# Performance work log

Hardware: AMD Instinct MI355X
Metric: run time of the kernel (lower is better)

Reference implementation:

```python
import jax, jax.numpy as jnp
import numpy as np
import math

B, L, C, H = 8, 1024, 1024, 8
EPS = 1e-5

def setup_inputs() -> dict:
    key = jax.random.key(0)
    ks = jax.random.split(key, 5)
    s = 0.02
    return {
        "x": jax.random.normal(ks[0], (B, L, C), dtype=jnp.float32),
        "ln_g": jnp.ones((C,), dtype=jnp.float32),
        "ln_b": jnp.zeros((C,), dtype=jnp.float32),
        "w_qkv": jax.random.normal(ks[1], (C, 3 * C), dtype=jnp.float32) * s,
        "b_qkv": jax.random.normal(ks[2], (3 * C,), dtype=jnp.float32) * s,
        "w_out": jax.random.normal(ks[3], (C, C), dtype=jnp.float32) * s,
        "b_out": jax.random.normal(ks[4], (C,), dtype=jnp.float32) * s,
    }

def reference(x, ln_g, ln_b, w_qkv, b_qkv, w_out, b_out):
    bs, length, width = x.shape
    ch = width // H
    # LayerNorm over channels
    mu = jnp.mean(x, axis=-1, keepdims=True)
    var = jnp.mean(jnp.square(x - mu), axis=-1, keepdims=True)
    xn = (x - mu) * jax.lax.rsqrt(var + EPS) * ln_g + ln_b
    # fused QKV projection
    qkv = jnp.einsum('blc,cd->bld', xn, w_qkv) + b_qkv  # [B, L, 3C]
    q, k, v = jnp.split(qkv, 3, axis=2)                 # each [B, L, C]
    scale = 1.0 / math.sqrt(math.sqrt(ch))
    # faithful raw row-major reshape as in the torch .view call
    q = (q * scale).reshape(bs * H, length, ch)
    k = (k * scale).reshape(bs * H, length, ch)
    v = v.reshape(bs * H, length, ch)
    w = jnp.einsum('bqc,bkc->bqk', q, k)                # [B*H, L, L] score matrix
    w = jax.nn.softmax(w.astype(jnp.float32), axis=-1).astype(q.dtype)
    attn = jnp.einsum('bqk,bkc->bqc', w, v).reshape(bs, length, -1)
    out = jnp.einsum('blc,cd->bld', attn, w_out) + b_out + xn  # residual uses normalized x
    return out
```

## Files before the change

### kernel.cpp

```cpp
#include <hip/hip_runtime.h>
#include <hip/hip_bf16.h>


typedef __attribute__((ext_vector_type(8))) short short8;
typedef __attribute__((ext_vector_type(4))) float f32x4;

#define QK_SCALE 0.29730177875068026f

__device__ __forceinline__ float bf2f(ushort u) {
    union { float f; unsigned int i; } c; c.i = ((unsigned int)u) << 16; return c.f;
}
__device__ __forceinline__ ushort f2bf(float f) {
    union { float f; unsigned int i; } c; c.f = f;
    unsigned int x = c.i;
    return (ushort)((x + 0x7FFFu + ((x >> 16) & 1u)) >> 16);
}

__device__ __forceinline__ void gload_lds16(const ushort* g, ushort* l) {
    __builtin_amdgcn_global_load_lds(
        (const __attribute__((address_space(1))) unsigned int*)g,
        (__attribute__((address_space(3))) unsigned int*)l, 16, 0, 0);
}

__global__ __launch_bounds__(256) void ln_kernel(
    const float* __restrict__ x, const float* __restrict__ g,
    const float* __restrict__ b, ushort* __restrict__ xn) {
    int row = blockIdx.x;
    int tid = threadIdx.x;
    const float* xr = x + (size_t)row * 1024;
    float4 v4 = *(const float4*)(xr + tid * 4);
    float v[4] = {v4.x, v4.y, v4.z, v4.w};
    float s1 = 0.f, s2 = 0.f;
#pragma unroll
    for (int j = 0; j < 4; j++) { s1 += v[j]; s2 += v[j] * v[j]; }
#pragma unroll
    for (int m = 32; m >= 1; m >>= 1) { s1 += __shfl_xor(s1, m); s2 += __shfl_xor(s2, m); }
    __shared__ float r1[4], r2[4];
    int lane = tid & 63, w = tid >> 6;
    if (lane == 0) { r1[w] = s1; r2[w] = s2; }
    __syncthreads();
    s1 = r1[0] + r1[1] + r1[2] + r1[3];
    s2 = r2[0] + r2[1] + r2[2] + r2[3];
    float mu = s1 * (1.0f / 1024.0f);
    float var = s2 * (1.0f / 1024.0f) - mu * mu;
    float rs = rsqrtf(var + 1e-5f);
    int c0 = tid * 4;
    float4 gg = *(const float4*)(g + c0);
    float4 bb = *(const float4*)(b + c0);
    float gA[4] = {gg.x, gg.y, gg.z, gg.w};
    float bA[4] = {bb.x, bb.y, bb.z, bb.w};
    ushort o[4];
#pragma unroll
    for (int j = 0; j < 4; j++) o[j] = f2bf((v[j] - mu) * rs * gA[j] + bA[j]);
    uint2 pk;
    pk.x = (uint)o[0] | ((uint)o[1] << 16);
    pk.y = (uint)o[2] | ((uint)o[3] << 16);
    *(uint2*)(xn + (size_t)row * 1024 + c0) = pk;
}

__global__ __launch_bounds__(256) void transpose_kernel(
    const float* __restrict__ in, ushort* __restrict__ out, int R, int Cc) {
    __shared__ ushort t[32][33];
    int bx = blockIdx.x * 32, by = blockIdx.y * 32;
    int tx = threadIdx.x & 31, ty = threadIdx.x >> 5;
#pragma unroll
    for (int j = 0; j < 32; j += 8)
        t[ty + j][tx] = f2bf(in[(size_t)(by + ty + j) * Cc + bx + tx]);
    __syncthreads();
#pragma unroll
    for (int j = 0; j < 32; j += 8)
        out[(size_t)(bx + ty + j) * R + by + tx] = t[tx][ty + j];
}

__global__ __launch_bounds__(256) void transpose_head(
    const ushort* __restrict__ in, ushort* __restrict__ out) {
    __shared__ ushort t[32][33];
    int h = blockIdx.z;
    int j0 = blockIdx.y * 32;
    int d0 = blockIdx.x * 32;
    int tx = threadIdx.x & 31, ty = threadIdx.x >> 5;
    const ushort* src = in + (size_t)h * 131072;
    ushort* dst = out + (size_t)h * 131072;
#pragma unroll
    for (int j = 0; j < 32; j += 8)
        t[ty + j][tx] = src[(size_t)(j0 + ty + j) * 128 + d0 + tx];
    __syncthreads();
#pragma unroll
    for (int j = 0; j < 32; j += 8)
        dst[(size_t)(d0 + ty + j) * 1024 + j0 + tx] = t[tx][ty + j];
}

__global__ __launch_bounds__(256) void gemm_qkv(
    const ushort* __restrict__ A, const ushort* __restrict__ Bt,
    const float* __restrict__ bias, ushort* __restrict__ out0,
    ushort* __restrict__ out1, ushort* __restrict__ out2) {
    const int K = 1024;
    __shared__ __align__(16) ushort As[128 * 64];
    __shared__ __align__(16) ushort Bs[128 * 64];

    int tid = threadIdx.x;
    int lane = tid & 63, w = tid >> 6;
    int l15 = lane & 15, q4 = lane >> 4;
    int wr = (w >> 1) * 64, wc = (w & 1) * 64;
    int rowBase = blockIdx.y * 128, colBase = blockIdx.x * 128;

    f32x4 acc[4][4];
    f32x4 zero = {0.f, 0.f, 0.f, 0.f};
#pragma unroll
    for (int mi = 0; mi < 4; mi++)
#pragma unroll
        for (int ni = 0; ni < 4; ni++) acc[mi][ni] = zero;

    for (int kt = 0; kt < 16; kt++) {
        __syncthreads();
#pragma unroll
        for (int i = 0; i < 4; i++) {
            int linear = i * 256 + w * 64 + lane;
            int r = linear >> 3, p = linear & 7;
            int l = p ^ (r & 7);
            gload_lds16(&A[(size_t)(rowBase + r) * K + kt * 64 + l * 8], &As[linear * 8]);
            gload_lds16(&Bt[(size_t)(colBase + r) * K + kt * 64 + l * 8], &Bs[linear * 8]);
        }
        __syncthreads();

#pragma unroll
        for (int kk = 0; kk < 2; kk++) {
            short8 aF[4], bF[4];
#pragma unroll
            for (int mi = 0; mi < 4; mi++) {
                int r = wr + mi * 16 + l15;
                aF[mi] = *(const short8*)&As[r * 64 + ((kk * 4 + q4) ^ (r & 7)) * 8];
            }
#pragma unroll
            for (int ni = 0; ni < 4; ni++) {
                int r = wc + ni * 16 + l15;
                bF[ni] = *(const short8*)&Bs[r * 64 + ((kk * 4 + q4) ^ (r & 7)) * 8];
            }
#pragma unroll
            for (int mi = 0; mi < 4; mi++)
#pragma unroll
                for (int ni = 0; ni < 4; ni++)
                    acc[mi][ni] = __builtin_amdgcn_mfma_f32_16x16x32_bf16(
                        aF[mi], bF[ni], acc[mi][ni], 0, 0, 0);
        }
    }

#pragma unroll
    for (int mi = 0; mi < 4; mi++)
#pragma unroll
        for (int ni = 0; ni < 4; ni++) {
            f32x4 a = acc[mi][ni];
            int col = colBase + wc + ni * 16 + l15;
            float bv = bias[col];
#pragma unroll
            for (int r = 0; r < 4; r++) {
                int row = rowBase + wr + mi * 16 + q4 * 4 + r;
                float val = a[r] + bv;
                if (col < 2048) val *= QK_SCALE;
                int bsel = col >> 10, cc = col & 1023;
                ushort* dst = (bsel == 0) ? out0 : ((bsel == 1) ? out1 : out2);
                dst[(size_t)row * 1024 + cc] = f2bf(val);
            }
        }
}

__global__ __launch_bounds__(256, 4) void gemm_out(
    const ushort* __restrict__ A, const ushort* __restrict__ Bt,
    const float* __restrict__ bias, const ushort* __restrict__ resid,
    float* __restrict__ outf) {
    const int K = 1024;
    __shared__ __align__(16) ushort As[64 * 64];
    __shared__ __align__(16) ushort Bs[128 * 64];

    int tid = threadIdx.x;
    int lane = tid & 63, w = tid >> 6;
    int l15 = lane & 15, q4 = lane >> 4;
    int wr = (w >> 1) * 32, wc = (w & 1) * 64;
    int rowBase = blockIdx.y * 64, colBase = blockIdx.x * 128;

    f32x4 acc[2][4];
    f32x4 zero = {0.f, 0.f, 0.f, 0.f};
#pragma unroll
    for (int mi = 0; mi < 2; mi++)
#pragma unroll
        for (int ni = 0; ni < 4; ni++) acc[mi][ni] = zero;

    for (int kt = 0; kt < 16; kt++) {
        __syncthreads();
#pragma unroll
        for (int i = 0; i < 6; i++) {
            int id = i * 256 + w * 64 + lane;
            if (id < 512) {
                int r = id >> 3, p = id & 7;
                int l = p ^ (r & 7);
                gload_lds16(&A[(size_t)(rowBase + r) * K + kt * 64 + l * 8], &As[id * 8]);
            } else {
                int idb = id - 512;
                int r = idb >> 3, p = idb & 7;
                int l = p ^ (r & 7);
                gload_lds16(&Bt[(size_t)(colBase + r) * K + kt * 64 + l * 8], &Bs[idb * 8]);
            }
        }
        __syncthreads();

#pragma unroll
        for (int kk = 0; kk < 2; kk++) {
            short8 aF[2], bF[4];
#pragma unroll
            for (int mi = 0; mi < 2; mi++) {
                int r = wr + mi * 16 + l15;
                aF[mi] = *(const short8*)&As[r * 64 + ((kk * 4 + q4) ^ (r & 7)) * 8];
            }
#pragma unroll
            for (int ni = 0; ni < 4; ni++) {
                int r = wc + ni * 16 + l15;
                bF[ni] = *(const short8*)&Bs[r * 64 + ((kk * 4 + q4) ^ (r & 7)) * 8];
            }
#pragma unroll
            for (int mi = 0; mi < 2; mi++)
#pragma unroll
                for (int ni = 0; ni < 4; ni++)
                    acc[mi][ni] = __builtin_amdgcn_mfma_f32_16x16x32_bf16(
                        aF[mi], bF[ni], acc[mi][ni], 0, 0, 0);
        }
    }

#pragma unroll
    for (int mi = 0; mi < 2; mi++)
#pragma unroll
        for (int ni = 0; ni < 4; ni++) {
            f32x4 a = acc[mi][ni];
            int col = colBase + wc + ni * 16 + l15;
            float bv = bias[col];
#pragma unroll
            for (int r = 0; r < 4; r++) {
                int row = rowBase + wr + mi * 16 + q4 * 4 + r;
                float val = a[r] + bv + bf2f(resid[(size_t)row * 1024 + col]);
                outf[(size_t)row * 1024 + col] = val;
            }
        }
}

__global__ __launch_bounds__(256, 4) void attn_kernel(
    const ushort* __restrict__ qb, const ushort* __restrict__ kb,
    const ushort* __restrict__ vt, ushort* __restrict__ ob) {
    int g = blockIdx.x >> 4;
    int qblk = blockIdx.x & 15;
    const ushort* Qh = qb + (size_t)g * 131072;
    const ushort* Kh = kb + (size_t)g * 131072;
    const ushort* Vh = vt + (size_t)g * 131072;

    __shared__ __align__(16) ushort Ks[64 * 128];
    __shared__ __align__(16) ushort Vt[128 * 64];
    __shared__ __align__(16) ushort Ps[64 * 64];

    int tid = threadIdx.x, lane = tid & 63, w = tid >> 6;
    int l15 = lane & 15, q4 = lane >> 4;
    int q0 = qblk * 64;

    short8 qf[4];
#pragma unroll
    for (int ks = 0; ks < 4; ks++)
        qf[ks] = *(const short8*)&Qh[(size_t)(q0 + w * 16 + l15) * 128 + ks * 32 + q4 * 8];

    f32x4 zero = {0.f, 0.f, 0.f, 0.f};
    f32x4 o[8];
#pragma unroll
    for (int ni = 0; ni < 8; ni++) o[ni] = zero;
    float plsum[4] = {0.f, 0.f, 0.f, 0.f};

    for (int kt = 0; kt < 16; kt++) {
        __syncthreads();
#pragma unroll
        for (int i = 0; i < 4; i++) {
            int linear = i * 256 + w * 64 + lane;
            int r = linear >> 4, p = linear & 15;
            int l = p ^ (r & 15);
            gload_lds16(&Kh[(size_t)(kt * 64 + r) * 128 + l * 8], &Ks[linear * 8]);
        }
#pragma unroll
        for (int i = 0; i < 4; i++) {
            int id = i * 256 + tid;
            int d = id >> 3, c = id & 7;
            int pc = c ^ (d & 7);
            *(uint4*)&Vt[d * 64 + pc * 8] =
                *(const uint4*)&Vh[(size_t)d * 1024 + kt * 64 + c * 8];
        }
        __syncthreads();

        f32x4 sacc[4];
#pragma unroll
        for (int ni = 0; ni < 4; ni++) sacc[ni] = zero;
#pragma unroll
        for (int ks = 0; ks < 4; ks++) {
#pragma unroll
            for (int ni = 0; ni < 4; ni++) {
                int r = ni * 16 + l15;
                int p = (ks * 4 + q4) ^ (r & 15);
                short8 bF = *(const short8*)&Ks[r * 128 + p * 8];
                sacc[ni] = __builtin_amdgcn_mfma_f32_16x16x32_bf16(
                    qf[ks], bF, sacc[ni], 0, 0, 0);
            }
        }

#pragma unroll
        for (int ni = 0; ni < 4; ni++) {
#pragma unroll
            for (int r = 0; r < 4; r++) {
                float pv = __expf(sacc[ni][r]);
                plsum[r] += pv;
                int qloc = w * 16 + q4 * 4 + r;
                int key = ni * 16 + l15;
                int pc = (key >> 3) ^ (qloc & 7);
                Ps[qloc * 64 + pc * 8 + (key & 7)] = f2bf(pv);
            }
        }

#pragma unroll
        for (int ks2 = 0; ks2 < 2; ks2++) {
            int c = ks2 * 4 + q4;
            short8 aF = *(const short8*)&Ps[(w * 16 + l15) * 64 + (c ^ (l15 & 7)) * 8];
#pragma unroll
            for (int ni = 0; ni < 8; ni++) {
                int d = ni * 16 + l15;
                short8 bF = *(const short8*)&Vt[d * 64 + (c ^ (d & 7)) * 8];
                o[ni] = __builtin_amdgcn_mfma_f32_16x16x32_bf16(aF, bF, o[ni], 0, 0, 0);
            }
        }
    }

#pragma unroll
    for (int r = 0; r < 4; r++) {
#pragma unroll
        for (int m = 1; m < 16; m <<= 1) plsum[r] += __shfl_xor(plsum[r], m, 16);
    }
    float inv[4];
#pragma unroll
    for (int r = 0; r < 4; r++) inv[r] = 1.0f / plsum[r];
#pragma unroll
    for (int ni = 0; ni < 8; ni++)
#pragma unroll
        for (int r = 0; r < 4; r++) {
            int qrow = q0 + w * 16 + q4 * 4 + r;
            ob[(size_t)g * 131072 + (size_t)qrow * 128 + ni * 16 + l15] =
                f2bf(o[ni][r] * inv[r]);
        }
}

extern "C" void kernel_launch(void* const* d_in, const int* in_sizes, int n_in,
                              void* d_out, int out_size, void* d_ws, size_t ws_size,
                              hipStream_t stream) {
    const float* x     = (const float*)d_in[0];
    const float* ln_g  = (const float*)d_in[1];
    const float* ln_b  = (const float*)d_in[2];
    const float* w_qkv = (const float*)d_in[3];
    const float* b_qkv = (const float*)d_in[4];
    const float* w_out = (const float*)d_in[5];
    const float* b_out = (const float*)d_in[6];
    float* out = (float*)d_out;

    const size_t MC = 8192ull * 1024ull;
    ushort* xn    = (ushort*)d_ws;
    ushort* wqkvT = xn + MC;
    ushort* woutT = wqkvT + 3072ull * 1024ull;
    ushort* qbuf  = woutT + 1024ull * 1024ull;
    ushort* kbuf  = qbuf + MC;
    ushort* vtbuf = kbuf + MC;
    ushort* attnb = vtbuf + MC;

    ln_kernel<<<8192, 256, 0, stream>>>(x, ln_g, ln_b, xn);
    transpose_kernel<<<dim3(96, 32), 256, 0, stream>>>(w_qkv, wqkvT, 1024, 3072);
    transpose_kernel<<<dim3(32, 32), 256, 0, stream>>>(w_out, woutT, 1024, 1024);
    gemm_qkv<<<dim3(24, 64), 256, 0, stream>>>(xn, wqkvT, b_qkv, qbuf, kbuf, attnb);
    transpose_head<<<dim3(4, 32, 64), 256, 0, stream>>>(attnb, vtbuf);
    attn_kernel<<<1024, 256, 0, stream>>>(qbuf, kbuf, vtbuf, attnb);
    gemm_out<<<dim3(8, 128), 256, 0, stream>>>(attnb, woutT, b_out, xn, out);
}
```

Before: 268.4 us.

## Merge prep kernels, hoist GEMM load addresses, and give attention warps two query tiles

Folds the LayerNorm and both weight transposes into a single prep launch that dispatches on block index. In both GEMMs, the global-to-LDS source and destination pointers are computed once and advanced per k-step, and the epilogue loops are reordered so bias and scale are loaded once per column. The attention kernel drops to 128 threads per block, with each warp owning 32 query rows as two 16-row tiles, so each K and V fragment read from LDS feeds two MFMAs. The trade-off is more accumulator registers per thread and fewer warps per block to hide latency.

```diff
diff --git a/kernel.cpp b/kernel.cpp
--- a/kernel.cpp
+++ b/kernel.cpp
@@ -22,54 +22,65 @@
         (__attribute__((address_space(3))) unsigned int*)l, 16, 0, 0);
 }
 
-__global__ __launch_bounds__(256) void ln_kernel(
+__global__ __launch_bounds__(256) void prep_kernel(
     const float* __restrict__ x, const float* __restrict__ g,
-    const float* __restrict__ b, ushort* __restrict__ xn) {
-    int row = blockIdx.x;
+    const float* __restrict__ b, ushort* __restrict__ xn,
+    const float* __restrict__ w_qkv, ushort* __restrict__ wqkvT,
+    const float* __restrict__ w_out, ushort* __restrict__ woutT) {
+    __shared__ float r1[4], r2[4];
+    __shared__ ushort t[32][33];
+    int bid = blockIdx.x;
     int tid = threadIdx.x;
-    const float* xr = x + (size_t)row * 1024;
-    float4 v4 = *(const float4*)(xr + tid * 4);
-    float v[4] = {v4.x, v4.y, v4.z, v4.w};
-    float s1 = 0.f, s2 = 0.f;
-#pragma unroll
-    for (int j = 0; j < 4; j++) { s1 += v[j]; s2 += v[j] * v[j]; }
-#pragma unroll
-    for (int m = 32; m >= 1; m >>= 1) { s1 += __shfl_xor(s1, m); s2 += __shfl_xor(s2, m); }
-    __shared__ float r1[4], r2[4];
-    int lane = tid & 63, w = tid >> 6;
-    if (lane == 0) { r1[w] = s1; r2[w] = s2; }
-    __syncthreads();
-    s1 = r1[0] + r1[1] + r1[2] + r1[3];
-    s2 = r2[0] + r2[1] + r2[2] + r2[3];
-    float mu = s1 * (1.0f / 1024.0f);
-    float var = s2 * (1.0f / 1024.0f) - mu * mu;
-    float rs = rsqrtf(var + 1e-5f);
-    int c0 = tid * 4;
-    float4 gg = *(const float4*)(g + c0);
-    float4 bb = *(const float4*)(b + c0);
-    float gA[4] = {gg.x, gg.y, gg.z, gg.w};
-    float bA[4] = {bb.x, bb.y, bb.z, bb.w};
-    ushort o[4];
-#pragma unroll
-    for (int j = 0; j < 4; j++) o[j] = f2bf((v[j] - mu) * rs * gA[j] + bA[j]);
-    uint2 pk;
-    pk.x = (uint)o[0] | ((uint)o[1] << 16);
-    pk.y = (uint)o[2] | ((uint)o[3] << 16);
-    *(uint2*)(xn + (size_t)row * 1024 + c0) = pk;
-}
-
-__global__ __launch_bounds__(256) void transpose_kernel(
-    const float* __restrict__ in, ushort* __restrict__ out, int R, int Cc) {
-    __shared__ ushort t[32][33];
-    int bx = blockIdx.x * 32, by = blockIdx.y * 32;
-    int tx = threadIdx.x & 31, ty = threadIdx.x >> 5;
-#pragma unroll
-    for (int j = 0; j < 32; j += 8)
-        t[ty + j][tx] = f2bf(in[(size_t)(by + ty + j) * Cc + bx + tx]);
-    __syncthreads();
-#pragma unroll
-    for (int j = 0; j < 32; j += 8)
-        out[(size_t)(bx + ty + j) * R + by + tx] = t[tx][ty + j];
+    if (bid < 8192) {
+        int row = bid;
+        const float* xr = x + (size_t)row * 1024;
+        float4 v4 = *(const float4*)(xr + tid * 4);
+        float v[4] = {v4.x, v4.y, v4.z, v4.w};
+        float s1 = 0.f, s2 = 0.f;
+#pragma unroll
+        for (int j = 0; j < 4; j++) { s1 += v[j]; s2 += v[j] * v[j]; }
+#pragma unroll
+        for (int m = 32; m >= 1; m >>= 1) { s1 += __shfl_xor(s1, m); s2 += __shfl_xor(s2, m); }
+        int lane = tid & 63, w = tid >> 6;
+        if (lane == 0) { r1[w] = s1; r2[w] = s2; }
+        __syncthreads();
+        s1 = r1[0] + r1[1] + r1[2] + r1[3];
+        s2 = r2[0] + r2[1] + r2[2] + r2[3];
+        float mu = s1 * (1.0f / 1024.0f);
+        float var = s2 * (1.0f / 1024.0f) - mu * mu;
+        float rs = rsqrtf(var + 1e-5f);
+        int c0 = tid * 4;
+        float4 gg = *(const float4*)(g + c0);
+        float4 bb = *(const float4*)(b + c0);
+        float gA[4] = {gg.x, gg.y, gg.z, gg.w};
+        float bA[4] = {bb.x, bb.y, bb.z, bb.w};
+        ushort o[4];
+#pragma unroll
+        for (int j = 0; j < 4; j++) o[j] = f2bf((v[j] - mu) * rs * gA[j] + bA[j]);
+        uint2 pk;
+        pk.x = (uint)o[0] | ((uint)o[1] << 16);
+        pk.y = (uint)o[2] | ((uint)o[3] << 16);
+        *(uint2*)(xn + (size_t)row * 1024 + c0) = pk;
+    } else {
+        const float* in; ushort* out; int R, Cc, bx, by;
+        if (bid < 11264) {
+            int tt = bid - 8192;
+            in = w_qkv; out = wqkvT; R = 1024; Cc = 3072;
+            bx = (tt % 96) * 32; by = (tt / 96) * 32;
+        } else {
+            int tt = bid - 11264;
+            in = w_out; out = woutT; R = 1024; Cc = 1024;
+            bx = (tt % 32) * 32; by = (tt / 32) * 32;
+        }
+        int tx = tid & 31, ty = tid >> 5;
+#pragma unroll
+        for (int j = 0; j < 32; j += 8)
+            t[ty + j][tx] = f2bf(in[(size_t)(by + ty + j) * Cc + bx + tx]);
+        __syncthreads();
+#pragma unroll
+        for (int j = 0; j < 32; j += 8)
+            out[(size_t)(bx + ty + j) * R + by + tx] = t[tx][ty + j];
+    }
 }
 
 __global__ __launch_bounds__(256) void transpose_head(
@@ -104,6 +115,19 @@
     int wr = (w >> 1) * 64, wc = (w & 1) * 64;
     int rowBase = blockIdx.y * 128, colBase = blockIdx.x * 128;
 
+    const ushort* aS[4]; const ushort* bS[4];
+    ushort* aD[4]; ushort* bD[4];
+#pragma unroll
+    for (int i = 0; i < 4; i++) {
+        int linear = i * 256 + w * 64 + lane;
+        int r = linear >> 3;
+        int l = (linear & 7) ^ (r & 7);
+        aS[i] = A + (size_t)(rowBase + r) * K + l * 8;
+        bS[i] = Bt + (size_t)(colBase + r) * K + l * 8;
+        aD[i] = &As[linear * 8];
+        bD[i] = &Bs[linear * 8];
+    }
+
     f32x4 acc[4][4];
     f32x4 zero = {0.f, 0.f, 0.f, 0.f};
 #pragma unroll
@@ -115,11 +139,9 @@
         __syncthreads();
 #pragma unroll
         for (int i = 0; i < 4; i++) {
-            int linear = i * 256 + w * 64 + lane;
-            int r = linear >> 3, p = linear & 7;
-            int l = p ^ (r & 7);
-            gload_lds16(&A[(size_t)(rowBase + r) * K + kt * 64 + l * 8], &As[linear * 8]);
-            gload_lds16(&Bt[(size_t)(colBase + r) * K + kt * 64 + l * 8], &Bs[linear * 8]);
+            gload_lds16(aS[i], aD[i]);
+            gload_lds16(bS[i], bD[i]);
+            aS[i] += 64; bS[i] += 64;
         }
         __syncthreads();
 
@@ -146,22 +168,22 @@
     }
 
 #pragma unroll
-    for (int mi = 0; mi < 4; mi++)
-#pragma unroll
-        for (int ni = 0; ni < 4; ni++) {
+    for (int ni = 0; ni < 4; ni++) {
+        int col = colBase + wc + ni * 16 + l15;
+        float bv = bias[col];
+        float sc = (col < 2048) ? QK_SCALE : 1.0f;
+        int bsel = col >> 10, cc = col & 1023;
+        ushort* dst = (bsel == 0) ? out0 : ((bsel == 1) ? out1 : out2);
+#pragma unroll
+        for (int mi = 0; mi < 4; mi++) {
             f32x4 a = acc[mi][ni];
-            int col = colBase + wc + ni * 16 + l15;
-            float bv = bias[col];
 #pragma unroll
             for (int r = 0; r < 4; r++) {
                 int row = rowBase + wr + mi * 16 + q4 * 4 + r;
-                float val = a[r] + bv;
-                if (col < 2048) val *= QK_SCALE;
-                int bsel = col >> 10, cc = col & 1023;
-                ushort* dst = (bsel == 0) ? out0 : ((bsel == 1) ? out1 : out2);
-                dst[(size_t)row * 1024 + cc] = f2bf(val);
-            }
-        }
+                dst[(size_t)row * 1024 + cc] = f2bf((a[r] + bv) * sc);
+            }
+        }
+    }
 }
 
 __global__ __launch_bounds__(256, 4) void gemm_out(
@@ -178,6 +200,22 @@
     int wr = (w >> 1) * 32, wc = (w & 1) * 64;
     int rowBase = blockIdx.y * 64, colBase = blockIdx.x * 128;
 
+    const ushort* src[6]; ushort* dstp[6];
+#pragma unroll
+    for (int i = 0; i < 6; i++) {
+        int id = i * 256 + w * 64 + lane;
+        if (id < 512) {
+            int r = id >> 3, l = (id & 7) ^ ((id >> 3) & 7);
+            src[i] = A + (size_t)(rowBase + r) * K + l * 8;
+            dstp[i] = &As[id * 8];
+        } else {
+            int idb = id - 512;
+            int r = idb >> 3, l = (idb & 7) ^ ((idb >> 3) & 7);
+            src[i] = Bt + (size_t)(colBase + r) * K + l * 8;
+            dstp[i] = &Bs[idb * 8];
+        }
+    }
+
     f32x4 acc[2][4];
     f32x4 zero = {0.f, 0.f, 0.f, 0.f};
 #pragma unroll
@@ -189,17 +227,8 @@
         __syncthreads();
 #pragma unroll
         for (int i = 0; i < 6; i++) {
-            int id = i * 256 + w * 64 + lane;
-            if (id < 512) {
-                int r = id >> 3, p = id & 7;
-                int l = p ^ (r & 7);
-                gload_lds16(&A[(size_t)(rowBase + r) * K + kt * 64 + l * 8], &As[id * 8]);
-            } else {
-                int idb = id - 512;
-                int r = idb >> 3, p = idb & 7;
-                int l = p ^ (r & 7);
-                gload_lds16(&Bt[(size_t)(colBase + r) * K + kt * 64 + l * 8], &Bs[idb * 8]);
-            }
+            gload_lds16(src[i], dstp[i]);
+            src[i] += 64;
         }
         __syncthreads();
 
@@ -226,22 +255,23 @@
     }
 
 #pragma unroll
-    for (int mi = 0; mi < 2; mi++)
-#pragma unroll
-        for (int ni = 0; ni < 4; ni++) {
+    for (int ni = 0; ni < 4; ni++) {
+        int col = colBase + wc + ni * 16 + l15;
+        float bv = bias[col];
+#pragma unroll
+        for (int mi = 0; mi < 2; mi++) {
             f32x4 a = acc[mi][ni];
-            int col = colBase + wc + ni * 16 + l15;
-            float bv = bias[col];
 #pragma unroll
             for (int r = 0; r < 4; r++) {
                 int row = rowBase + wr + mi * 16 + q4 * 4 + r;
-                float val = a[r] + bv + bf2f(resid[(size_t)row * 1024 + col]);
-                outf[(size_t)row * 1024 + col] = val;
-            }
-        }
-}
-
-__global__ __launch_bounds__(256, 4) void attn_kernel(
+                outf[(size_t)row * 1024 + col] =
+                    a[r] + bv + bf2f(resid[(size_t)row * 1024 + col]);
+            }
+        }
+    }
+}
+
+__global__ __launch_bounds__(128, 2) void attn_kernel(
     const ushort* __restrict__ qb, const ushort* __restrict__ kb,
     const ushort* __restrict__ vt, ushort* __restrict__ ob) {
     int g = blockIdx.x >> 4;
@@ -258,29 +288,34 @@
     int l15 = lane & 15, q4 = lane >> 4;
     int q0 = qblk * 64;
 
-    short8 qf[4];
-#pragma unroll
-    for (int ks = 0; ks < 4; ks++)
-        qf[ks] = *(const short8*)&Qh[(size_t)(q0 + w * 16 + l15) * 128 + ks * 32 + q4 * 8];
+    short8 qf[2][4];
+#pragma unroll
+    for (int mi = 0; mi < 2; mi++)
+#pragma unroll
+        for (int ks = 0; ks < 4; ks++)
+            qf[mi][ks] = *(const short8*)
+                &Qh[(size_t)(q0 + w * 32 + mi * 16 + l15) * 128 + ks * 32 + q4 * 8];
 
     f32x4 zero = {0.f, 0.f, 0.f, 0.f};
-    f32x4 o[8];
-#pragma unroll
-    for (int ni = 0; ni < 8; ni++) o[ni] = zero;
-    float plsum[4] = {0.f, 0.f, 0.f, 0.f};
+    f32x4 o[2][8];
+#pragma unroll
+    for (int mi = 0; mi < 2; mi++)
+#pragma unroll
+        for (int ni = 0; ni < 8; ni++) o[mi][ni] = zero;
+    float plsum[2][4] = {{0.f, 0.f, 0.f, 0.f}, {0.f, 0.f, 0.f, 0.f}};
 
     for (int kt = 0; kt < 16; kt++) {
         __syncthreads();
 #pragma unroll
-        for (int i = 0; i < 4; i++) {
-            int linear = i * 256 + w * 64 + lane;
+        for (int i = 0; i < 8; i++) {
+            int linear = i * 128 + w * 64 + lane;
             int r = linear >> 4, p = linear & 15;
             int l = p ^ (r & 15);
             gload_lds16(&Kh[(size_t)(kt * 64 + r) * 128 + l * 8], &Ks[linear * 8]);
         }
 #pragma unroll
-        for (int i = 0; i < 4; i++) {
-            int id = i * 256 + tid;
+        for (int i = 0; i < 8; i++) {
+            int id = i * 128 + tid;
             int d = id >> 3, c = id & 7;
             int pc = c ^ (d & 7);
             *(uint4*)&Vt[d * 64 + pc * 8] =
@@ -288,63 +323,85 @@
         }
         __syncthreads();
 
-        f32x4 sacc[4];
-#pragma unroll
-        for (int ni = 0; ni < 4; ni++) sacc[ni] = zero;
+        f32x4 sacc[2][4];
+#pragma unroll
+        for (int mi = 0; mi < 2; mi++)
+#pragma unroll
+            for (int ni = 0; ni < 4; ni++) sacc[mi][ni] = zero;
 #pragma unroll
         for (int ks = 0; ks < 4; ks++) {
+            short8 bF[4];
 #pragma unroll
             for (int ni = 0; ni < 4; ni++) {
                 int r = ni * 16 + l15;
                 int p = (ks * 4 + q4) ^ (r & 15);
-                short8 bF = *(const short8*)&Ks[r * 128 + p * 8];
-                sacc[ni] = __builtin_amdgcn_mfma_f32_16x16x32_bf16(
-                    qf[ks], bF, sacc[ni], 0, 0, 0);
-            }
-        }
-
-#pragma unroll
-        for (int ni = 0; ni < 4; ni++) {
-#pragma unroll
-            for (int r = 0; r < 4; r++) {
-                float pv = __expf(sacc[ni][r]);
-                plsum[r] += pv;
-                int qloc = w * 16 + q4 * 4 + r;
-                int key = ni * 16 + l15;
-                int pc = (key >> 3) ^ (qloc & 7);
-                Ps[qloc * 64 + pc * 8 + (key & 7)] = f2bf(pv);
-            }
-        }
-
-#pragma unroll
-        for (int ks2 = 0; ks2 < 2; ks2++) {
-            int c = ks2 * 4 + q4;
-            short8 aF = *(const short8*)&Ps[(w * 16 + l15) * 64 + (c ^ (l15 & 7)) * 8];
+                bF[ni] = *(const short8*)&Ks[r * 128 + p * 8];
+            }
+#pragma unroll
+            for (int mi = 0; mi < 2; mi++)
+#pragma unroll
+                for (int ni = 0; ni < 4; ni++)
+                    sacc[mi][ni] = __builtin_amdgcn_mfma_f32_16x16x32_bf16(
+                        qf[mi][ks], bF[ni], sacc[mi][ni], 0, 0, 0);
+        }
+
+#pragma unroll
+        for (int mi = 0; mi < 2; mi++)
+#pragma unroll
+            for (int ni = 0; ni < 4; ni++)
+#pragma unroll
+                for (int r = 0; r < 4; r++) {
+                    float pv = __expf(sacc[mi][ni][r]);
+                    plsum[mi][r] += pv;
+                    int qloc = w * 32 + mi * 16 + q4 * 4 + r;
+                    int key = ni * 16 + l15;
+                    int pc = (key >> 3) ^ (qloc & 7);
+                    Ps[qloc * 64 + pc * 8 + (key & 7)] = f2bf(pv);
+                }
+
+#pragma unroll
+        for (int kb2 = 0; kb2 < 2; kb2++) {
+            int c = kb2 * 4 + q4;
+            short8 aF[2];
+#pragma unroll
+            for (int mi = 0; mi < 2; mi++) {
+                int row = w * 32 + mi * 16 + l15;
+                aF[mi] = *(const short8*)&Ps[row * 64 + (c ^ (l15 & 7)) * 8];
+            }
 #pragma unroll
             for (int ni = 0; ni < 8; ni++) {
                 int d = ni * 16 + l15;
                 short8 bF = *(const short8*)&Vt[d * 64 + (c ^ (d & 7)) * 8];
-                o[ni] = __builtin_amdgcn_mfma_f32_16x16x32_bf16(aF, bF, o[ni], 0, 0, 0);
-            }
-        }
-    }
-
-#pragma unroll
-    for (int r = 0; r < 4; r++) {
-#pragma unroll
-        for (int m = 1; m < 16; m <<= 1) plsum[r] += __shfl_xor(plsum[r], m, 16);
-    }
-    float inv[4];
-#pragma unroll
-    for (int r = 0; r < 4; r++) inv[r] = 1.0f / plsum[r];
-#pragma unroll
-    for (int ni = 0; ni < 8; ni++)
+#pragma unroll
+                for (int mi = 0; mi < 2; mi++)
+                    o[mi][ni] = __builtin_amdgcn_mfma_f32_16x16x32_bf16(
+                        aF[mi], bF, o[mi][ni], 0, 0, 0);
+            }
+        }
+    }
+
+#pragma unroll
+    for (int mi = 0; mi < 2; mi++)
 #pragma unroll
         for (int r = 0; r < 4; r++) {
-            int qrow = q0 + w * 16 + q4 * 4 + r;
-            ob[(size_t)g * 131072 + (size_t)qrow * 128 + ni * 16 + l15] =
-                f2bf(o[ni][r] * inv[r]);
-        }
+#pragma unroll
+            for (int m = 1; m < 16; m <<= 1)
+                plsum[mi][r] += __shfl_xor(plsum[mi][r], m, 16);
+        }
+#pragma unroll
+    for (int mi = 0; mi < 2; mi++) {
+        float inv[4];
+#pragma unroll
+        for (int r = 0; r < 4; r++) inv[r] = 1.0f / plsum[mi][r];
+#pragma unroll
+        for (int ni = 0; ni < 8; ni++)
+#pragma unroll
+            for (int r = 0; r < 4; r++) {
+                int qrow = q0 + w * 32 + mi * 16 + q4 * 4 + r;
+                ob[(size_t)g * 131072 + (size_t)qrow * 128 + ni * 16 + l15] =
+                    f2bf(o[mi][ni][r] * inv[r]);
+            }
+    }
 }
 
 extern "C" void kernel_launch(void* const* d_in, const int* in_sizes, int n_in,
@@ -368,11 +425,9 @@
     ushort* vtbuf = kbuf + MC;
     ushort* attnb = vtbuf + MC;
 
-    ln_kernel<<<8192, 256, 0, stream>>>(x, ln_g, ln_b, xn);
-    transpose_kernel<<<dim3(96, 32), 256, 0, stream>>>(w_qkv, wqkvT, 1024, 3072);
-    transpose_kernel<<<dim3(32, 32), 256, 0, stream>>>(w_out, woutT, 1024, 1024);
+    prep_kernel<<<12288, 256, 0, stream>>>(x, ln_g, ln_b, xn, w_qkv, wqkvT, w_out, woutT);
     gemm_qkv<<<dim3(24, 64), 256, 0, stream>>>(xn, wqkvT, b_qkv, qbuf, kbuf, attnb);
     transpose_head<<<dim3(4, 32, 64), 256, 0, stream>>>(attnb, vtbuf);
-    attn_kernel<<<1024, 256, 0, stream>>>(qbuf, kbuf, vtbuf, attnb);
+    attn_kernel<<<1024, 128, 0, stream>>>(qbuf, kbuf, vtbuf, attnb);
     gemm_out<<<dim3(8, 128), 256, 0, stream>>>(attnb, woutT, b_out, xn, out);
 }
```

New measurement: 264.9 us. Within noise of the previous version (-1.3%).
